# Performance work log

Hardware: AMD Instinct MI355X
Metric: run time of the kernel (lower is better)

The kernel has to match this reference:

```python
import math
import jax, jax.numpy as jnp
import numpy as np

B, L, D, H, INNER = 8, 1024, 256, 8, 1024
HD = D // H
EPS = 1e-12


def _ln(x, g, b):
    m = jnp.mean(x, axis=-1, keepdims=True)
    v = jnp.mean((x - m) ** 2, axis=-1, keepdims=True)
    return (x - m) / jnp.sqrt(v + EPS) * g + b


def setup_inputs() -> dict:
    key = jax.random.key(0)
    ks = jax.random.split(key, 16)
    def lin(k, out_d, in_d):
        s = 1.0 / math.sqrt(in_d)
        kw, kb = jax.random.split(k)
        return (jax.random.uniform(kw, (out_d, in_d), jnp.float32, -s, s),
                jax.random.uniform(kb, (out_d,), jnp.float32, -s, s))
    Wq, bq = lin(ks[0], D, D)
    Wk, bk = lin(ks[1], D, D)
    Wv, bv = lin(ks[2], D, D)
    Wo, bo = lin(ks[3], D, D)
    W1, b1 = lin(ks[4], INNER, D)
    W2, b2 = lin(ks[5], D, INNER)
    return {
        'hidden_states': jax.random.normal(ks[6], (B, L, D), jnp.float32),
        'attention_mask': jnp.zeros((B, 1, 1, L), jnp.float32),
        'phi': jax.random.uniform(ks[7], (B, H, L), jnp.float32, 0.0, 2.0 * math.pi),
        'mag': jax.random.uniform(ks[8], (B, H, L), jnp.float32),
        'Wq': Wq, 'bq': bq, 'Wk': Wk, 'bk': bk, 'Wv': Wv, 'bv': bv,
        'Wo': Wo, 'bo': bo,
        'ln1_g': jnp.ones((D,), jnp.float32), 'ln1_b': jnp.zeros((D,), jnp.float32),
        'gamma': jnp.full((1, H, 1, 1), 0.1, jnp.float32),
        'W1': W1, 'b1': b1, 'W2': W2, 'b2': b2,
        'ln2_g': jnp.ones((D,), jnp.float32), 'ln2_b': jnp.zeros((D,), jnp.float32),
    }


def reference(hidden_states, attention_mask, phi, mag, Wq, bq, Wk, bk, Wv, bv,
              Wo, bo, ln1_g, ln1_b, gamma, W1, b1, W2, b2, ln2_g, ln2_b):
    residual = hidden_states
    def shape(x):  # [B,L,D] -> [B,H,L,hd]
        return x.reshape(B, L, H, HD).transpose(0, 2, 1, 3)
    q = shape(hidden_states @ Wq.T + bq)
    k = shape(hidden_states @ Wk.T + bk)
    v = shape(hidden_states @ Wv.T + bv)
    semantic = jnp.einsum('bhld,bhmd->bhlm', q, k) / math.sqrt(HD)
    # physics: gamma * (mag_i*mag_j) * cos(phi_i - phi_j), per band/head
    physics = gamma * (mag[..., :, None] * mag[..., None, :]) * jnp.cos(phi[..., :, None] - phi[..., None, :])
    scores = semantic + physics + attention_mask
    eye = jnp.eye(L, dtype=bool)[None, None]
    row_max = jnp.max(scores, axis=-1, keepdims=True)
    scores = jnp.where(row_max <= -1e8, jnp.where(eye, 0.0, scores), scores)
    probs = jax.nn.softmax(scores, axis=-1)
    ctx = jnp.einsum('bhlm,bhmd->bhld', probs, v).transpose(0, 2, 1, 3).reshape(B, L, D)
    attn_out = _ln(ctx @ Wo.T + bo + residual, ln1_g, ln1_b)
    h = attn_out @ W1.T + b1
    h = h * 0.5 * (1.0 + jax.lax.erf(h / math.sqrt(2.0)))  # exact-erf gelu as in source
    return _ln(h @ W2.T + b2 + attn_out, ln2_g, ln2_b)
```

## Files before the change

kernel.cpp:

```cpp
#include <hip/hip_runtime.h>
#include <hip/hip_bf16.h>
#include <math.h>

typedef __attribute__((ext_vector_type(8))) short bf16x8;
typedef __attribute__((ext_vector_type(4))) float f32x4;
typedef __attribute__((ext_vector_type(16))) float f32x16;

__device__ __forceinline__ unsigned short f2bf(float f) {
  union { float f; unsigned u; } v; v.f = f;
  unsigned r = v.u + 0x7fffu + ((v.u >> 16) & 1u);
  return (unsigned short)(r >> 16);
}
__device__ __forceinline__ unsigned pack2(float lo, float hi) {
  return (unsigned)f2bf(lo) | ((unsigned)f2bf(hi) << 16);
}
__device__ __forceinline__ float bf2f(unsigned short u) {
  union { unsigned u; float f; } v; v.u = ((unsigned)u) << 16; return v.f;
}
__device__ __forceinline__ float fexp2(float x) {
#if __has_builtin(__builtin_amdgcn_exp2f)
  return __builtin_amdgcn_exp2f(x);
#else
  return exp2f(x);
#endif
}
__device__ __forceinline__ unsigned cvtpk(float lo, float hi) {
  unsigned r;
  asm("v_cvt_pk_bf16_f32 %0, %1, %2" : "=v"(r) : "v"(lo), "v"(hi));
  return r;
}
__device__ __forceinline__ void gload16(const void* gsrc, void* lds) {
  __builtin_amdgcn_global_load_lds(
      (const __attribute__((address_space(1))) unsigned int*)gsrc,
      (__attribute__((address_space(3))) unsigned int*)lds, 16, 0, 0);
}
#if __has_builtin(__builtin_amdgcn_permlane32_swap)
typedef __attribute__((ext_vector_type(2))) unsigned u32x2;
__device__ __forceinline__ void plswap(unsigned& a, unsigned& b) {
  u32x2 r = __builtin_amdgcn_permlane32_swap(a, b, false, false);
  a = r[0]; b = r[1];
}
#else
__device__ __forceinline__ void plswap(unsigned& a, unsigned& b) {
  unsigned as = (unsigned)__shfl_xor((int)a, 32, 64);
  unsigned bs = (unsigned)__shfl_xor((int)b, 32, 64);
  bool hi = (threadIdx.x & 32) != 0;
  unsigned na = hi ? bs : a;
  unsigned nb = hi ? b : as;
  a = na; b = nb;
}
#endif

#define L2E 1.4426950408889634f

__device__ __forceinline__ int xcd_swz(int p, int cpx) {
  return (p & 7) * cpx + (p >> 3);
}

__global__ __launch_bounds__(256) void prep_kernel(
    const float* __restrict__ hs, const float* __restrict__ phi,
    const float* __restrict__ mag, const float* __restrict__ mask,
    const float* __restrict__ gamma, const float* __restrict__ Wq,
    const float* __restrict__ Wk, const float* __restrict__ Wv,
    const float* __restrict__ Wo, const float* __restrict__ W1,
    const float* __restrict__ W2, unsigned short* __restrict__ wts,
    unsigned short* __restrict__ hsb, unsigned short* __restrict__ qx,
    unsigned short* __restrict__ kx) {
  const int blk = blockIdx.x, tid = threadIdx.x;
  if (blk < 768) {
    int i = blk * 1024 + tid * 4;
    const float* src; int off;
    if (i < 262144) {
      src = (i < 131072) ? (i < 65536 ? Wq : Wk) : (i < 196608 ? Wv : Wo);
      off = i & 65535;
    } else if (i < 524288) { src = W1; off = i - 262144; }
    else { src = W2; off = i - 524288; }
    float4 v = *(const float4*)&src[off];
    *(uint2*)&wts[i] = make_uint2(pack2(v.x, v.y), pack2(v.z, v.w));
  } else if (blk < 1792) {
    int i = (blk - 768) * 2048 + tid * 8;
    const float4* hp = (const float4*)hs;
    float4 a = hp[i >> 2], b = hp[(i >> 2) + 1];
    uint4 o = make_uint4(pack2(a.x, a.y), pack2(a.z, a.w), pack2(b.x, b.y),
                         pack2(b.z, b.w));
    *(uint4*)&hsb[i] = o;
  } else {
    int row = (blk - 1792) * 256 + tid;
    int bh = row >> 10, key = row & 1023, b = row >> 13, h = (row >> 10) & 7;
    float p = phi[row], mg = mag[row];
    float sn, cs; sincosf(p, &sn, &cs);
    float c = mg * cs, s = mg * sn;
    float msk = mask[b * 1024 + key];
    int ch = key >> 5, k32 = key & 31;
    size_t base = ((((size_t)(bh * 32 + ch) * 3 + 2) * 2 + 0) * 32 + k32) * 8;
    *(uint4*)&kx[base] = make_uint4(pack2(c, s), pack2(msk, 0.0f), 0u, 0u);
    *(uint4*)&kx[base + 256] = make_uint4(0u, 0u, 0u, 0u);
    float g = gamma[h];
    *(uint4*)&qx[base] = make_uint4(pack2(L2E * g * c, L2E * g * s),
                                    pack2(L2E, 0.0f), 0u, 0u);
    *(uint4*)&qx[base + 256] = make_uint4(0u, 0u, 0u, 0u);
  }
}

__global__ __launch_bounds__(256) void gemm_qkv(
    const unsigned short* __restrict__ A, const unsigned short* __restrict__ wts,
    const float* __restrict__ bq, const float* __restrict__ bk,
    const float* __restrict__ bv, unsigned short* __restrict__ qx,
    unsigned short* __restrict__ kx, unsigned short* __restrict__ vt2) {
  __shared__ __align__(16) unsigned short As[128 * 64];
  __shared__ __align__(16) unsigned short Bs[128 * 64];
  const int tid = threadIdx.x;
  const int w_id = xcd_swz(blockIdx.x, 48);
  const int xw = w_id % 6;
  const int mat = xw >> 1;
  const int n0 = (xw & 1) * 128;
  const int m0 = (w_id / 6) * 128;
  const unsigned short* W = wts + mat * 65536;
  const float* bias = (mat == 0) ? bq : ((mat == 1) ? bk : bv);
  const int wm = (tid >> 7) & 1, wn = (tid >> 6) & 1;
  const int g = (tid >> 4) & 3, c = tid & 15;
  const int l = tid & 63, wv = tid >> 6;
  const int rr = l >> 3, scol = ((l & 7) ^ rr) << 3;
  const unsigned short* aSrc = &A[(size_t)(m0 + wv * 32 + rr) * 256 + scol];
  const unsigned short* bSrc = &W[(size_t)(n0 + wv * 32 + rr) * 256 + scol];
  unsigned short* aDst = &As[wv * 32 * 64];
  unsigned short* bDst = &Bs[wv * 32 * 64];
  f32x4 acc[4][4] = {};
  for (int k0 = 0; k0 < 256; k0 += 64) {
    __syncthreads();
#pragma unroll
    for (int i = 0; i < 4; i++) {
      gload16(aSrc + (size_t)i * 8 * 256 + k0, aDst + i * 8 * 64);
      gload16(bSrc + (size_t)i * 8 * 256 + k0, bDst + i * 8 * 64);
    }
    __syncthreads();
#pragma unroll
    for (int kk = 0; kk < 2; kk++) {
      bf16x8 af[4], bfr[4];
#pragma unroll
      for (int mi = 0; mi < 4; mi++) {
        int row = wm * 64 + mi * 16 + c;
        af[mi] = *(const bf16x8*)&As[row * 64 + (((g + 4 * kk) ^ (row & 7)) << 3)];
      }
#pragma unroll
      for (int ni = 0; ni < 4; ni++) {
        int row = wn * 64 + ni * 16 + c;
        bfr[ni] = *(const bf16x8*)&Bs[row * 64 + (((g + 4 * kk) ^ (row & 7)) << 3)];
      }
#pragma unroll
      for (int mi = 0; mi < 4; mi++)
#pragma unroll
        for (int ni = 0; ni < 4; ni++)
          acc[mi][ni] = __builtin_amdgcn_mfma_f32_16x16x32_bf16(af[mi], bfr[ni], acc[mi][ni], 0, 0, 0);
    }
  }
  const float scale = (mat == 0) ? (L2E * 0.17677669529663687f) : 1.0f;
#pragma unroll
  for (int ni = 0; ni < 4; ni++) {
    int n = n0 + wn * 64 + ni * 16 + c;
    float bv_ = bias[n];
    int h = n >> 5, dd = n & 31;
#pragma unroll
    for (int mi = 0; mi < 4; mi++) {
      int mbase = m0 + wm * 64 + mi * 16 + 4 * g;
      int bb = mbase >> 10, rowL = mbase & 1023;
      int bh = bb * 8 + h;
      if (mat < 2) {
        unsigned short* out = (mat == 0) ? qx : kx;
        int m_idx = dd >> 4, hi = (dd >> 3) & 1, j = dd & 7;
#pragma unroll
        for (int r = 0; r < 4; r++) {
          int keyL = rowL + r;
          int ch = keyL >> 5, k32 = keyL & 31;
          out[(((((size_t)bh * 32 + ch) * 3 + m_idx) * 2 + hi) * 32 + k32) * 8 + j] =
              f2bf((acc[mi][ni][r] + bv_) * scale);
        }
      } else {
        int keyL = rowL;
        int ch = keyL >> 5, t = (keyL >> 4) & 1, hi = (keyL >> 3) & 1;
        size_t base = (((((size_t)bh * 32 + ch) * 2 + t) * 2 + hi) * 32 + dd) * 8 + (g & 1) * 4;
        uint2 w2 = make_uint2(pack2(acc[mi][ni][0] + bv_, acc[mi][ni][1] + bv_),
                              pack2(acc[mi][ni][2] + bv_, acc[mi][ni][3] + bv_));
        *(uint2*)&vt2[base] = w2;
      }
    }
  }
}

__global__ __launch_bounds__(256) void attn32(
    const unsigned short* __restrict__ qx, const unsigned short* __restrict__ kx,
    const unsigned short* __restrict__ vt2, unsigned short* __restrict__ ctx) {
  const int tid = threadIdx.x;
  const int wave = tid >> 6, lane = tid & 63;
  const int hi = lane >> 5, l31 = lane & 31;
  const int w_id = xcd_swz(blockIdx.x, 64);
  const int bh = w_id >> 3, bb = bh >> 3, h = bh & 7;
  const int qch = (w_id & 7) * 4 + wave;

  const size_t qoff = (((size_t)(bh * 32 + qch) * 3 * 2 + hi) * 32 + l31) * 8;
  bf16x8 qf0 = *(const bf16x8*)&qx[qoff];
  bf16x8 qf1 = *(const bf16x8*)&qx[qoff + 512];
  bf16x8 qf2 = *(const bf16x8*)&qx[qoff + 1024];

  f32x16 acc = {};
  float mrun = 0.0f, lsum = 0.0f;

  for (int ch = 0; ch < 32; ch++) {
    const size_t koff = (((size_t)(bh * 32 + ch) * 3 * 2 + hi) * 32 + l31) * 8;
    bf16x8 kf0 = *(const bf16x8*)&kx[koff];
    bf16x8 kf1 = *(const bf16x8*)&kx[koff + 512];
    bf16x8 kf2 = *(const bf16x8*)&kx[koff + 1024];
    const size_t voff = (((size_t)(bh * 32 + ch) * 2 * 2 + hi) * 32 + l31) * 8;
    bf16x8 vf0 = *(const bf16x8*)&vt2[voff];
    bf16x8 vf1 = *(const bf16x8*)&vt2[voff + 512];

    f32x16 s = {};
    s = __builtin_amdgcn_mfma_f32_32x32x16_bf16(kf0, qf0, s, 0, 0, 0);
    s = __builtin_amdgcn_mfma_f32_32x32x16_bf16(kf1, qf1, s, 0, 0, 0);
    s = __builtin_amdgcn_mfma_f32_32x32x16_bf16(kf2, qf2, s, 0, 0, 0);

    float pm = fmaxf(fmaxf(fmaxf(s[0], s[1]), fmaxf(s[2], s[3])),
                     fmaxf(fmaxf(s[4], s[5]), fmaxf(s[6], s[7])));
    pm = fmaxf(pm, fmaxf(fmaxf(fmaxf(s[8], s[9]), fmaxf(s[10], s[11])),
                         fmaxf(fmaxf(s[12], s[13]), fmaxf(s[14], s[15]))));
    pm = fmaxf(pm, __shfl_xor(pm, 32, 64));
    if (__any(pm > mrun + 12.0f)) {
      float mn = fmaxf(mrun, pm);
      float rs = fexp2(mrun - mn);
      lsum *= rs;
      mrun = mn;
#pragma unroll
      for (int r = 0; r < 16; r++) {
        float rr = __shfl(rs, (r & 3) + 8 * (r >> 2) + 4 * hi, 64);
        acc[r] *= rr;
      }
    }
    float p[16];
#pragma unroll
    for (int r = 0; r < 16; r++) p[r] = fexp2(s[r] - mrun);
    lsum += (((p[0] + p[1]) + (p[2] + p[3])) + ((p[4] + p[5]) + (p[6] + p[7]))) +
            (((p[8] + p[9]) + (p[10] + p[11])) + ((p[12] + p[13]) + (p[14] + p[15])));
    unsigned u0 = cvtpk(p[0], p[1]), u1 = cvtpk(p[2], p[3]);
    unsigned u2 = cvtpk(p[4], p[5]), u3 = cvtpk(p[6], p[7]);
    plswap(u0, u2); plswap(u1, u3);
    unsigned u4 = cvtpk(p[8], p[9]), u5 = cvtpk(p[10], p[11]);
    unsigned u6 = cvtpk(p[12], p[13]), u7 = cvtpk(p[14], p[15]);
    plswap(u4, u6); plswap(u5, u7);
    union { unsigned u[4]; bf16x8 v; } A1, A2;
    A1.u[0] = u0; A1.u[1] = u1; A1.u[2] = u2; A1.u[3] = u3;
    A2.u[0] = u4; A2.u[1] = u5; A2.u[2] = u6; A2.u[3] = u7;
    acc = __builtin_amdgcn_mfma_f32_32x32x16_bf16(A1.v, vf0, acc, 0, 0, 0);
    acc = __builtin_amdgcn_mfma_f32_32x32x16_bf16(A2.v, vf1, acc, 0, 0, 0);
  }
  lsum += __shfl_xor(lsum, 32, 64);
  float inv = 1.0f / lsum;
#pragma unroll
  for (int r = 0; r < 16; r++) {
    int qr = (r & 3) + 8 * (r >> 2) + 4 * hi;
    float rr = __shfl(inv, qr, 64);
    ctx[((size_t)bb * 1024 + qch * 32 + qr) * 256 + h * 32 + l31] = f2bf(acc[r] * rr);
  }
}

template <int EPI, int NB>
__global__ __launch_bounds__(256) void gemm64(
    const unsigned short* __restrict__ A, const unsigned short* __restrict__ W,
    const float* __restrict__ bias, const void* __restrict__ resid,
    float* __restrict__ Cout, int N, int K) {
  __shared__ __align__(16) unsigned short As[64 * 64];
  __shared__ __align__(16) unsigned short Bs[64 * 64];
  const int tid = threadIdx.x;
  const int w_id = xcd_swz(blockIdx.x, (NB * 128) / 8);
  const int n0 = (w_id % NB) * 64;
  const int m0 = (w_id / NB) * 64;
  const int wm = (tid >> 7) & 1, wn = (tid >> 6) & 1;
  const int g = (tid >> 4) & 3, c = tid & 15;
  const int l = tid & 63, wv = tid >> 6;
  const int rr = l >> 3, scol = ((l & 7) ^ rr) << 3;
  const unsigned short* aSrc = &A[(size_t)(m0 + wv * 16 + rr) * K + scol];
  const unsigned short* bSrc = &W[(size_t)(n0 + wv * 16 + rr) * K + scol];
  unsigned short* aDst = &As[wv * 16 * 64];
  unsigned short* bDst = &Bs[wv * 16 * 64];
  f32x4 acc[2][2] = {};
  for (int k0 = 0; k0 < K; k0 += 64) {
    __syncthreads();
#pragma unroll
    for (int i = 0; i < 2; i++) {
      gload16(aSrc + (size_t)i * 8 * K + k0, aDst + i * 8 * 64);
      gload16(bSrc + (size_t)i * 8 * K + k0, bDst + i * 8 * 64);
    }
    __syncthreads();
#pragma unroll
    for (int kk = 0; kk < 2; kk++) {
      bf16x8 af[2], bfr[2];
#pragma unroll
      for (int mi = 0; mi < 2; mi++) {
        int row = wm * 32 + mi * 16 + c;
        af[mi] = *(const bf16x8*)&As[row * 64 + (((g + 4 * kk) ^ (row & 7)) << 3)];
      }
#pragma unroll
      for (int ni = 0; ni < 2; ni++) {
        int row = wn * 32 + ni * 16 + c;
        bfr[ni] = *(const bf16x8*)&Bs[row * 64 + (((g + 4 * kk) ^ (row & 7)) << 3)];
      }
#pragma unroll
      for (int mi = 0; mi < 2; mi++)
#pragma unroll
        for (int ni = 0; ni < 2; ni++)
          acc[mi][ni] = __builtin_amdgcn_mfma_f32_16x16x32_bf16(af[mi], bfr[ni], acc[mi][ni], 0, 0, 0);
    }
  }
#pragma unroll
  for (int ni = 0; ni < 2; ni++) {
    int n = n0 + wn * 32 + ni * 16 + c;
    float bv_ = bias[n];
#pragma unroll
    for (int mi = 0; mi < 2; mi++) {
      int mbase = m0 + wm * 32 + mi * 16 + 4 * g;
#pragma unroll
      for (int r = 0; r < 4; r++) {
        int m = mbase + r;
        float x = acc[mi][ni][r] + bv_;
        if constexpr (EPI == 1)
          Cout[(size_t)m * N + n] = x + ((const float*)resid)[(size_t)m * N + n];
        else
          Cout[(size_t)m * N + n] =
              x + bf2f(((const unsigned short*)resid)[(size_t)m * N + n]);
      }
    }
  }
}

__global__ __launch_bounds__(256) void gemm_ffn1(
    const unsigned short* __restrict__ A, const unsigned short* __restrict__ W,
    const float* __restrict__ bias, unsigned short* __restrict__ Cout,
    int N, int K) {
  __shared__ __align__(16) unsigned short As[128 * 64];
  __shared__ __align__(16) unsigned short Bs[128 * 64];
  const int tid = threadIdx.x;
  const int w_id = xcd_swz(blockIdx.x, 64);
  const int n0 = (w_id % 8) * 128;
  const int m0 = (w_id / 8) * 128;
  const int wm = (tid >> 7) & 1, wn = (tid >> 6) & 1;
  const int g = (tid >> 4) & 3, c = tid & 15;
  const int l = tid & 63, wv = tid >> 6;
  const int rr = l >> 3, scol = ((l & 7) ^ rr) << 3;
  const unsigned short* aSrc = &A[(size_t)(m0 + wv * 32 + rr) * K + scol];
  const unsigned short* bSrc = &W[(size_t)(n0 + wv * 32 + rr) * K + scol];
  unsigned short* aDst = &As[wv * 32 * 64];
  unsigned short* bDst = &Bs[wv * 32 * 64];
  f32x4 acc[4][4] = {};
  for (int k0 = 0; k0 < K; k0 += 64) {
    __syncthreads();
#pragma unroll
    for (int i = 0; i < 4; i++) {
      gload16(aSrc + (size_t)i * 8 * K + k0, aDst + i * 8 * 64);
      gload16(bSrc + (size_t)i * 8 * K + k0, bDst + i * 8 * 64);
    }
    __syncthreads();
#pragma unroll
    for (int kk = 0; kk < 2; kk++) {
      bf16x8 af[4], bfr[4];
#pragma unroll
      for (int mi = 0; mi < 4; mi++) {
        int row = wm * 64 + mi * 16 + c;
        af[mi] = *(const bf16x8*)&As[row * 64 + (((g + 4 * kk) ^ (row & 7)) << 3)];
      }
#pragma unroll
      for (int ni = 0; ni < 4; ni++) {
        int row = wn * 64 + ni * 16 + c;
        bfr[ni] = *(const bf16x8*)&Bs[row * 64 + (((g + 4 * kk) ^ (row & 7)) << 3)];
      }
#pragma unroll
      for (int mi = 0; mi < 4; mi++)
#pragma unroll
        for (int ni = 0; ni < 4; ni++)
          acc[mi][ni] = __builtin_amdgcn_mfma_f32_16x16x32_bf16(af[mi], bfr[ni], acc[mi][ni], 0, 0, 0);
    }
  }
#pragma unroll
  for (int ni = 0; ni < 4; ni++) {
    int n = n0 + wn * 64 + ni * 16 + c;
    float bv_ = bias[n];
#pragma unroll
    for (int mi = 0; mi < 4; mi++) {
      int mbase = m0 + wm * 64 + mi * 16 + 4 * g;
#pragma unroll
      for (int r = 0; r < 4; r++) {
        int m = mbase + r;
        float x = acc[mi][ni][r] + bv_;
        Cout[(size_t)m * N + n] =
            f2bf(x * 0.5f * (1.0f + erff(x * 0.70710678118654752f)));
      }
    }
  }
}

template <int OUTBF>
__global__ __launch_bounds__(256) void ln_kernel(const float* __restrict__ x,
                                                 const float* __restrict__ g,
                                                 const float* __restrict__ b,
                                                 void* __restrict__ y) {
  const int lane = threadIdx.x & 63;
  const int row = blockIdx.x * 4 + (threadIdx.x >> 6);
  const float4 v = *(const float4*)&x[(size_t)row * 256 + lane * 4];
  float s1 = (v.x + v.y) + (v.z + v.w);
  float s2 = (v.x * v.x + v.y * v.y) + (v.z * v.z + v.w * v.w);
#pragma unroll
  for (int o = 1; o < 64; o <<= 1) {
    s1 += __shfl_xor(s1, o, 64);
    s2 += __shfl_xor(s2, o, 64);
  }
  float mean = s1 * (1.0f / 256.0f);
  float var = fmaxf(s2 * (1.0f / 256.0f) - mean * mean, 0.0f);
  float istd = rsqrtf(var + 1e-12f);
  float4 gv = *(const float4*)&g[lane * 4];
  float4 bv = *(const float4*)&b[lane * 4];
  float o0 = (v.x - mean) * istd * gv.x + bv.x;
  float o1 = (v.y - mean) * istd * gv.y + bv.y;
  float o2 = (v.z - mean) * istd * gv.z + bv.z;
  float o3 = (v.w - mean) * istd * gv.w + bv.w;
  if constexpr (OUTBF) {
    *(uint2*)&((unsigned short*)y)[(size_t)row * 256 + lane * 4] =
        make_uint2(pack2(o0, o1), pack2(o2, o3));
  } else {
    float4 o = make_float4(o0, o1, o2, o3);
    *(float4*)&((float*)y)[(size_t)row * 256 + lane * 4] = o;
  }
}

extern "C" void kernel_launch(void* const* d_in, const int* in_sizes, int n_in,
                              void* d_out, int out_size, void* d_ws,
                              size_t ws_size, hipStream_t stream) {
  const float* hs = (const float*)d_in[0];
  const float* mask = (const float*)d_in[1];
  const float* phi = (const float*)d_in[2];
  const float* mag = (const float*)d_in[3];
  const float* Wq = (const float*)d_in[4];
  const float* bq = (const float*)d_in[5];
  const float* Wk = (const float*)d_in[6];
  const float* bk = (const float*)d_in[7];
  const float* Wv = (const float*)d_in[8];
  const float* bv = (const float*)d_in[9];
  const float* Wo = (const float*)d_in[10];
  const float* bo = (const float*)d_in[11];
  const float* ln1g = (const float*)d_in[12];
  const float* ln1b = (const float*)d_in[13];
  const float* gamma = (const float*)d_in[14];
  const float* W1 = (const float*)d_in[15];
  const float* b1 = (const float*)d_in[16];
  const float* W2 = (const float*)d_in[17];
  const float* b2 = (const float*)d_in[18];
  const float* ln2g = (const float*)d_in[19];
  const float* ln2b = (const float*)d_in[20];

  char* wsb = (char*)d_ws;
  unsigned short* wts = (unsigned short*)(wsb + 0);
  unsigned short* hsb = (unsigned short*)(wsb + (2ull << 20));
  unsigned short* ctx = (unsigned short*)(wsb + (6ull << 20));
  unsigned short* aout = (unsigned short*)(wsb + (10ull << 20));
  float* tmp = (float*)(wsb + (14ull << 20));
  unsigned short* qx = (unsigned short*)(wsb + (22ull << 20));
  unsigned short* kx = (unsigned short*)(wsb + (28ull << 20));
  unsigned short* vt2 = (unsigned short*)(wsb + (34ull << 20));
  unsigned short* hbuf = (unsigned short*)(wsb + (22ull << 20));

  dim3 blk(256);
  prep_kernel<<<dim3(2048), blk, 0, stream>>>(hs, phi, mag, mask, gamma, Wq, Wk,
                                              Wv, Wo, W1, W2, wts, hsb, qx, kx);
  gemm_qkv<<<dim3(384), blk, 0, stream>>>(hsb, wts, bq, bk, bv, qx, kx, vt2);
  attn32<<<dim3(512), blk, 0, stream>>>(qx, kx, vt2, ctx);
  gemm64<1, 4><<<dim3(512), blk, 0, stream>>>(ctx, wts + 196608, bo, hs, tmp, 256, 256);
  ln_kernel<1><<<dim3(2048), blk, 0, stream>>>(tmp, ln1g, ln1b, aout);
  gemm_ffn1<<<dim3(512), blk, 0, stream>>>(aout, wts + 262144, b1, hbuf, 1024, 256);
  gemm64<3, 4><<<dim3(512), blk, 0, stream>>>(hbuf, wts + 524288, b2, aout, tmp, 256, 1024);
  ln_kernel<0><<<dim3(2048), blk, 0, stream>>>(tmp, ln2g, ln2b, d_out);
}
```

Baseline: 99.99 us.

## Fuse Wo projection with residual add and LayerNorm; raise MFMA priority in attention

Replaces the separate Wo GEMM plus LayerNorm kernels with one kernel. Each 512-thread block computes a full 16-row by 256-column output tile, adds bias and residual, reduces row statistics across waves through shared memory, and writes the normalized bf16 result directly. This removes the fp32 temporary round trip and one launch. The attention loop also wraps its MFMA groups in s_setprio so matrix instructions get issue priority over other waves. The cost is that each block reloads the full 256x256 Wo tile for only 16 rows, giving lower weight reuse per block.

```diff
diff --git a/kernel.cpp b/kernel.cpp
--- a/kernel.cpp
+++ b/kernel.cpp
@@ -215,9 +215,11 @@
     bf16x8 vf1 = *(const bf16x8*)&vt2[voff + 512];
 
     f32x16 s = {};
+    __builtin_amdgcn_s_setprio(1);
     s = __builtin_amdgcn_mfma_f32_32x32x16_bf16(kf0, qf0, s, 0, 0, 0);
     s = __builtin_amdgcn_mfma_f32_32x32x16_bf16(kf1, qf1, s, 0, 0, 0);
     s = __builtin_amdgcn_mfma_f32_32x32x16_bf16(kf2, qf2, s, 0, 0, 0);
+    __builtin_amdgcn_s_setprio(0);
 
     float pm = fmaxf(fmaxf(fmaxf(s[0], s[1]), fmaxf(s[2], s[3])),
                      fmaxf(fmaxf(s[4], s[5]), fmaxf(s[6], s[7])));
@@ -249,8 +251,10 @@
     union { unsigned u[4]; bf16x8 v; } A1, A2;
     A1.u[0] = u0; A1.u[1] = u1; A1.u[2] = u2; A1.u[3] = u3;
     A2.u[0] = u4; A2.u[1] = u5; A2.u[2] = u6; A2.u[3] = u7;
+    __builtin_amdgcn_s_setprio(1);
     acc = __builtin_amdgcn_mfma_f32_32x32x16_bf16(A1.v, vf0, acc, 0, 0, 0);
     acc = __builtin_amdgcn_mfma_f32_32x32x16_bf16(A2.v, vf1, acc, 0, 0, 0);
+    __builtin_amdgcn_s_setprio(0);
   }
   lsum += __shfl_xor(lsum, 32, 64);
   float inv = 1.0f / lsum;
@@ -259,6 +263,96 @@
     int qr = (r & 3) + 8 * (r >> 2) + 4 * hi;
     float rr = __shfl(inv, qr, 64);
     ctx[((size_t)bb * 1024 + qch * 32 + qr) * 256 + h * 32 + l31] = f2bf(acc[r] * rr);
+  }
+}
+
+__global__ __launch_bounds__(512) void wo_ln(
+    const unsigned short* __restrict__ A, const unsigned short* __restrict__ W,
+    const float* __restrict__ bias, const float* __restrict__ resid,
+    const float* __restrict__ lng, const float* __restrict__ lnb,
+    unsigned short* __restrict__ aout) {
+  __shared__ __align__(16) unsigned short As[16 * 64];
+  __shared__ __align__(16) unsigned short Bs[256 * 64];
+  __shared__ float red[2][8][16];
+  const int tid = threadIdx.x;
+  const int w_id = xcd_swz(blockIdx.x, 64);
+  const int m0 = w_id * 16;
+  const int w = tid >> 6, l = tid & 63;
+  const int g = (l >> 4) & 3, c = l & 15;
+  const int rr = l >> 3, scol = ((l & 7) ^ rr) << 3;
+  const unsigned short* aSrc = &A[(size_t)(m0 + rr) * 256 + scol];
+  const unsigned short* bSrc = &W[(size_t)(w * 32 + rr) * 256 + scol];
+  unsigned short* bDst = &Bs[w * 32 * 64];
+  f32x4 acc[2] = {};
+  for (int k0 = 0; k0 < 256; k0 += 64) {
+    __syncthreads();
+    if (w == 0) {
+      gload16(aSrc + k0, &As[0]);
+      gload16(aSrc + (size_t)8 * 256 + k0, &As[8 * 64]);
+    }
+#pragma unroll
+    for (int i = 0; i < 4; i++)
+      gload16(bSrc + (size_t)i * 8 * 256 + k0, bDst + i * 8 * 64);
+    __syncthreads();
+#pragma unroll
+    for (int kk = 0; kk < 2; kk++) {
+      bf16x8 af = *(const bf16x8*)&As[c * 64 + (((g + 4 * kk) ^ (c & 7)) << 3)];
+#pragma unroll
+      for (int ni = 0; ni < 2; ni++) {
+        int row = w * 32 + ni * 16 + c;
+        bf16x8 bfr = *(const bf16x8*)&Bs[row * 64 + (((g + 4 * kk) ^ (row & 7)) << 3)];
+        acc[ni] = __builtin_amdgcn_mfma_f32_16x16x32_bf16(af, bfr, acc[ni], 0, 0, 0);
+      }
+    }
+  }
+  float x[2][4], s1[4], s2[4];
+#pragma unroll
+  for (int r = 0; r < 4; r++) { s1[r] = 0.0f; s2[r] = 0.0f; }
+#pragma unroll
+  for (int ni = 0; ni < 2; ni++) {
+    int n = w * 32 + ni * 16 + c;
+    float bv_ = bias[n];
+#pragma unroll
+    for (int r = 0; r < 4; r++) {
+      int m = m0 + 4 * g + r;
+      float v = acc[ni][r] + bv_ + resid[(size_t)m * 256 + n];
+      x[ni][r] = v;
+      s1[r] += v;
+      s2[r] += v * v;
+    }
+  }
+#pragma unroll
+  for (int off = 1; off < 16; off <<= 1) {
+#pragma unroll
+    for (int r = 0; r < 4; r++) {
+      s1[r] += __shfl_xor(s1[r], off, 64);
+      s2[r] += __shfl_xor(s2[r], off, 64);
+    }
+  }
+  if (c == 0) {
+#pragma unroll
+    for (int r = 0; r < 4; r++) {
+      red[0][w][4 * g + r] = s1[r];
+      red[1][w][4 * g + r] = s2[r];
+    }
+  }
+  __syncthreads();
+#pragma unroll
+  for (int r = 0; r < 4; r++) {
+    int row = 4 * g + r;
+    float t1 = 0.0f, t2 = 0.0f;
+#pragma unroll
+    for (int ww = 0; ww < 8; ww++) { t1 += red[0][ww][row]; t2 += red[1][ww][row]; }
+    float mean = t1 * (1.0f / 256.0f);
+    float var = fmaxf(t2 * (1.0f / 256.0f) - mean * mean, 0.0f);
+    float istd = rsqrtf(var + 1e-12f);
+    int m = m0 + row;
+#pragma unroll
+    for (int ni = 0; ni < 2; ni++) {
+      int n = w * 32 + ni * 16 + c;
+      aout[(size_t)m * 256 + n] =
+          f2bf((x[ni][r] - mean) * istd * lng[n] + lnb[n]);
+    }
   }
 }
 
@@ -396,11 +490,10 @@
   }
 }
 
-template <int OUTBF>
 __global__ __launch_bounds__(256) void ln_kernel(const float* __restrict__ x,
                                                  const float* __restrict__ g,
                                                  const float* __restrict__ b,
-                                                 void* __restrict__ y) {
+                                                 float* __restrict__ y) {
   const int lane = threadIdx.x & 63;
   const int row = blockIdx.x * 4 + (threadIdx.x >> 6);
   const float4 v = *(const float4*)&x[(size_t)row * 256 + lane * 4];
@@ -416,17 +509,11 @@
   float istd = rsqrtf(var + 1e-12f);
   float4 gv = *(const float4*)&g[lane * 4];
   float4 bv = *(const float4*)&b[lane * 4];
-  float o0 = (v.x - mean) * istd * gv.x + bv.x;
-  float o1 = (v.y - mean) * istd * gv.y + bv.y;
-  float o2 = (v.z - mean) * istd * gv.z + bv.z;
-  float o3 = (v.w - mean) * istd * gv.w + bv.w;
-  if constexpr (OUTBF) {
-    *(uint2*)&((unsigned short*)y)[(size_t)row * 256 + lane * 4] =
-        make_uint2(pack2(o0, o1), pack2(o2, o3));
-  } else {
-    float4 o = make_float4(o0, o1, o2, o3);
-    *(float4*)&((float*)y)[(size_t)row * 256 + lane * 4] = o;
-  }
+  float4 o = make_float4((v.x - mean) * istd * gv.x + bv.x,
+                         (v.y - mean) * istd * gv.y + bv.y,
+                         (v.z - mean) * istd * gv.z + bv.z,
+                         (v.w - mean) * istd * gv.w + bv.w);
+  *(float4*)&y[(size_t)row * 256 + lane * 4] = o;
 }
 
 extern "C" void kernel_launch(void* const* d_in, const int* in_sizes, int n_in,
@@ -470,9 +557,9 @@
                                               Wv, Wo, W1, W2, wts, hsb, qx, kx);
   gemm_qkv<<<dim3(384), blk, 0, stream>>>(hsb, wts, bq, bk, bv, qx, kx, vt2);
   attn32<<<dim3(512), blk, 0, stream>>>(qx, kx, vt2, ctx);
-  gemm64<1, 4><<<dim3(512), blk, 0, stream>>>(ctx, wts + 196608, bo, hs, tmp, 256, 256);
-  ln_kernel<1><<<dim3(2048), blk, 0, stream>>>(tmp, ln1g, ln1b, aout);
+  wo_ln<<<dim3(512), dim3(512), 0, stream>>>(ctx, wts + 196608, bo, hs, ln1g,
+                                             ln1b, aout);
   gemm_ffn1<<<dim3(512), blk, 0, stream>>>(aout, wts + 262144, b1, hbuf, 1024, 256);
   gemm64<3, 4><<<dim3(512), blk, 0, stream>>>(hbuf, wts + 524288, b2, aout, tmp, 256, 1024);
-  ln_kernel<0><<<dim3(2048), blk, 0, stream>>>(tmp, ln2g, ln2b, d_out);
-}
+  ln_kernel<<<dim3(2048), blk, 0, stream>>>(tmp, ln2g, ln2b, (float*)d_out);
+}
```

New measurement: 94.01 us. 1.06x faster.
